# Performance work log

Measured on AMD Instinct MI355X. Metric: run time of the kernel, lower is better.

The kernel has to match this reference:

```python
import jax, jax.numpy as jnp
import numpy as np

B, T, D, H, LORA = 4, 1024, 1024, 16, 64
HD = D // H
BLOCK_ID, N_BLOCKS = 6, 12


def _ln(x, w, b, eps=1e-5):
    m = x.mean(-1, keepdims=True)
    v = ((x - m) ** 2).mean(-1, keepdims=True)
    return (x - m) * jax.lax.rsqrt(v + eps) * w + b


def _lora(z, a, b, l):
    return l + jnp.tanh(z @ a.T) @ b.T


def setup_inputs() -> dict:
    key = jax.random.key(0)
    ks = iter(jax.random.split(key, 64))
    rn = lambda shape, s: jax.random.normal(next(ks), shape, jnp.float32) * s
    inp = {}
    inp['x'] = rn((B, T, D), 1.0)
    r1 = 1.0 - BLOCK_ID / N_BLOCKS
    i = np.arange(D)
    inp['xw'] = jnp.asarray(1.0 - (i / D) ** r1, jnp.float32)
    for nm in ('rW', 'kW', 'vW', 'gW'):
        inp[nm] = rn((D, D), 0.02)
    for p in ('r', 'k', 'v', 'g', 'd'):
        inp[p + '_la'] = rn((LORA, D), 0.001)
        inp[p + '_lb'] = rn((D, LORA), 0.001)
        inp[p + '_ll'] = rn((D,), 1.0)
    inp['ln_w'] = jnp.full((HD,), ((1 + BLOCK_ID) / N_BLOCKS) ** 0.7, jnp.float32)
    inp['ln_b'] = jnp.zeros((HD,), jnp.float32)
    inp['oW'] = rn((D, D), 0.02)
    inp['init_state'] = rn((H, HD, HD), 1.0)
    r0 = BLOCK_ID / (N_BLOCKS - 1)
    ih = i % HD
    inp['u'] = jnp.asarray(r0 * (1 - ih / (D - 1)) + np.remainder(0.1 * (ih + 1), 3.0), jnp.float32)
    return inp


def reference(x, xw, rW, kW, vW, gW, r_la, r_lb, r_ll, k_la, k_lb, k_ll,
              v_la, v_lb, v_ll, g_la, g_lb, g_ll, d_la, d_lb, d_ll,
              ln_w, ln_b, oW, init_state, u):
    b, t, d = x.shape
    h = init_state.shape[0]
    hd = d // h
    # token shift: xx[t] = x[t-1], xx[0] = 0
    xx = jnp.concatenate([jnp.zeros_like(x[:, :1]), x[:, :-1]], axis=1)
    dx = xx - x
    lerpx = x + dx * xw
    r = (x + dx * _lora(lerpx, r_la, r_lb, r_ll)) @ rW.T
    k = (x + dx * _lora(lerpx, k_la, k_lb, k_ll)) @ kW.T
    v = (x + dx * _lora(lerpx, v_la, v_lb, v_ll)) @ vW.T
    g = (x + dx * _lora(lerpx, g_la, g_lb, g_ll)) @ gW.T
    w = jnp.exp(-jnp.exp(_lora(x + dx * _lora(lerpx, d_la, d_lb, d_ll), d_la, d_lb, d_ll)))
    # [B,T,D] -> [T,B,H,hd] for the time scan
    split = lambda z: z.reshape(b, t, h, hd).transpose(1, 0, 2, 3)
    rs, ws, ks, vs = split(r), split(w), split(k), split(v)
    uh = u.reshape(h, hd)
    st0 = jnp.broadcast_to(init_state, (b, h, hd, hd))

    def step(st, inp):
        rt, wt, kt, vt = inp
        kv = jnp.einsum('bhi,bhj->bhij', kt, vt)      # outer product
        y = jnp.einsum('bhi,bhij->bhj', rt, st + uh[None, :, :, None] * kv)
        return wt[..., None] * st + kv, y             # diag(w) @ S + kv

    st1, ys = jax.lax.scan(step, st0, (rs, ws, ks, vs))  # ys: [T,B,H,hd]
    o = jax.nn.silu(g.reshape(b, t, h, hd)) * _ln(ys.transpose(1, 0, 2, 3), ln_w, ln_b)
    return o.reshape(b, t, d) @ oW.T, st1
```

## Files before the change

### kernel.cpp

```cpp
#include <hip/hip_runtime.h>
#include <hip/hip_bf16.h>

typedef unsigned short u16;
typedef unsigned int u32;
typedef __attribute__((ext_vector_type(4))) float f32x4;
typedef __attribute__((ext_vector_type(8))) short s16x8;

#define AS1 __attribute__((address_space(1)))
#define AS3 __attribute__((address_space(3)))

#define NB 4
#define TTOK 1024
#define DD 1024
#define NH 16
#define HD 64
#define MT 4096
#define NCH 16
#define CLEN 64

static __device__ __forceinline__ float b2f(u16 u) {
  union { unsigned int u; float f; } c; c.u = ((unsigned int)u) << 16; return c.f;
}
static __device__ __forceinline__ float ubit(u32 u) {
  union { u32 u; float f; } c; c.u = u; return c.f;
}
static __device__ __forceinline__ u16 f2b(float f) {
  union { float f; unsigned int u; } c; c.f = f;
  return (u16)((c.u + 0x7fffu + ((c.u >> 16) & 1u)) >> 16);
}
static __device__ __forceinline__ void gload16(const u16* g, u16* l) {
  __builtin_amdgcn_global_load_lds((const AS1 u32*)g, (AS3 u32*)l, 16, 0, 0);
}
static __device__ __forceinline__ int swz(int lin) {
  return lin ^ (((lin >> 9) & 3) << 5) ^ (((lin >> 7) & 1) << 4);
}

__global__ __launch_bounds__(256) void convW(const float* __restrict__ s0, const float* __restrict__ s1,
                                             const float* __restrict__ s2, const float* __restrict__ s3,
                                             const float* __restrict__ s4, u16* __restrict__ dst) {
  long f = ((long)blockIdx.x * 256 + threadIdx.x) << 2;
  int sel = (int)(f >> 20);
  const float* s = sel == 0 ? s0 : sel == 1 ? s1 : sel == 2 ? s2 : sel == 3 ? s3 : s4;
  long off = f & 1048575;
  f32x4 v = *(const f32x4*)&s[off];
  ushort4 o; o.x = f2b(v[0]); o.y = f2b(v[1]); o.z = f2b(v[2]); o.w = f2b(v[3]);
  *(ushort4*)&dst[f] = o;
}

__global__ __launch_bounds__(256) void convLora(
    const float* a0, const float* a1, const float* a2, const float* a3, const float* a4,
    const float* b0, const float* b1, const float* b2, const float* b3, const float* b4,
    const float* l0, const float* l1, const float* l2, const float* l3, const float* l4,
    u16* __restrict__ laD, u16* __restrict__ lbD, float* __restrict__ llD) {
  long f = ((long)blockIdx.x * 256 + threadIdx.x) << 2;
  if (f < 327680) {
    int sel = (int)(f >> 16); long off = f & 65535;
    const float* s = sel == 0 ? a0 : sel == 1 ? a1 : sel == 2 ? a2 : sel == 3 ? a3 : a4;
    f32x4 v = *(const f32x4*)&s[off];
    ushort4 o; o.x = f2b(v[0]); o.y = f2b(v[1]); o.z = f2b(v[2]); o.w = f2b(v[3]);
    *(ushort4*)&laD[f] = o;
  } else if (f < 655360) {
    long g = f - 327680;
    int sel = (int)(g >> 16); long off = g & 65535;
    const float* s = sel == 0 ? b0 : sel == 1 ? b1 : sel == 2 ? b2 : sel == 3 ? b3 : b4;
    f32x4 v = *(const f32x4*)&s[off];
    ushort4 o; o.x = f2b(v[0]); o.y = f2b(v[1]); o.z = f2b(v[2]); o.w = f2b(v[3]);
    *(ushort4*)&lbD[g] = o;
  } else if (f < 660480) {
    long g = f - 655360;
    int sel = (int)(g >> 10); long off = g & 1023;
    const float* s = sel == 0 ? l0 : sel == 1 ? l1 : sel == 2 ? l2 : sel == 3 ? l3 : l4;
    *(f32x4*)&llD[g] = *(const f32x4*)&s[off];
  }
}

__global__ __launch_bounds__(256) void prep(const float* __restrict__ x, const float* __restrict__ xw,
                                            u16* __restrict__ lerpx, u16* __restrict__ xB,
                                            u16* __restrict__ dxB) {
  long f = ((long)blockIdx.x * 256 + threadIdx.x) << 2;
  int d = (int)(f & (DD - 1));
  int m = (int)(f >> 10);
  int t = m & (TTOK - 1);
  f32x4 xv = *(const f32x4*)&x[f];
  f32x4 xm = {};
  if (t > 0) xm = *(const f32x4*)&x[f - DD];
  f32x4 xwv = *(const f32x4*)&xw[d];
  f32x4 dx = xm - xv;
  f32x4 lp = xv + dx * xwv;
  ushort4 o; o.x = f2b(lp[0]); o.y = f2b(lp[1]); o.z = f2b(lp[2]); o.w = f2b(lp[3]);
  *(ushort4*)&lerpx[f] = o;
  ushort4 ox; ox.x = f2b(xv[0]); ox.y = f2b(xv[1]); ox.z = f2b(xv[2]); ox.w = f2b(xv[3]);
  *(ushort4*)&xB[f] = ox;
  ushort4 od; od.x = f2b(dx[0]); od.y = f2b(dx[1]); od.z = f2b(dx[2]); od.w = f2b(dx[3]);
  *(ushort4*)&dxB[f] = od;
}

template<int BM, int BN, int EPI>
__launch_bounds__(256)
__global__ void gemm2(const u16* __restrict__ Ab, long sAz,
                      const u16* __restrict__ Bb, long sBz,
                      void* __restrict__ Ob, long sOz,
                      const float* __restrict__ llb,
                      const u16* __restrict__ xB,
                      const u16* __restrict__ dxB,
                      int M, int N, int K) {
  __shared__ __align__(16) u16 As[BM * 64];
  __shared__ __align__(16) u16 Bs[BN * 64];
  const int z = blockIdx.z;
  const u16* A = Ab + (long)z * sAz;
  const u16* Bw = Bb + (long)z * sBz;
  const int m0 = blockIdx.y * BM;
  const int n0 = blockIdx.x * BN;
  const int tid = threadIdx.x;
  const int l = tid & 63;
  const int wv = tid >> 6;
  constexpr int WM = BM / 2, WN = BN / 2;
  constexpr int FM = WM / 16, FN = WN / 16;
  const int wm0 = (wv >> 1) * WM, wn0 = (wv & 1) * WN;
  const int lrow = l & 15, lk = (l >> 4) * 8;
  constexpr int GA = BM / 32, GB = BN / 32;
  int gA[GA], gB[GB];
#pragma unroll
  for (int q = 0; q < GA; ++q) {
    int d = (q * 256 + tid) * 16;
    int bb = swz(d);
    gA[q] = (m0 + (bb >> 7)) * K + ((bb & 127) >> 1);
  }
#pragma unroll
  for (int q = 0; q < GB; ++q) {
    int d = (q * 256 + tid) * 16;
    int bb = swz(d);
    gB[q] = (n0 + (bb >> 7)) * K + ((bb & 127) >> 1);
  }
  int aOff[FM][2], bOff[FN][2];
#pragma unroll
  for (int m = 0; m < FM; ++m)
#pragma unroll
    for (int kk = 0; kk < 2; ++kk)
      aOff[m][kk] = swz(((wm0 + m * 16 + lrow) << 7) + (kk << 6) + (lk << 1));
#pragma unroll
  for (int n = 0; n < FN; ++n)
#pragma unroll
    for (int kk = 0; kk < 2; ++kk)
      bOff[n][kk] = swz(((wn0 + n * 16 + lrow) << 7) + (kk << 6) + (lk << 1));
  f32x4 acc[FM][FN] = {};
  for (int k0 = 0; k0 < K; k0 += 64) {
    __syncthreads();
#pragma unroll
    for (int q = 0; q < GA; ++q)
      gload16(&A[(long)gA[q] + k0], (u16*)((char*)As + (q * 256 + tid) * 16));
#pragma unroll
    for (int q = 0; q < GB; ++q)
      gload16(&Bw[(long)gB[q] + k0], (u16*)((char*)Bs + (q * 256 + tid) * 16));
    __syncthreads();
#pragma unroll
    for (int kk = 0; kk < 2; ++kk) {
      s16x8 af[FM], bfr[FN];
#pragma unroll
      for (int m = 0; m < FM; ++m) af[m] = *(const s16x8*)((const char*)As + aOff[m][kk]);
#pragma unroll
      for (int n = 0; n < FN; ++n) bfr[n] = *(const s16x8*)((const char*)Bs + bOff[n][kk]);
#pragma unroll
      for (int m = 0; m < FM; ++m)
#pragma unroll
        for (int n = 0; n < FN; ++n)
          acc[m][n] = __builtin_amdgcn_mfma_f32_16x16x32_bf16(af[m], bfr[n], acc[m][n], 0, 0, 0);
    }
  }
#pragma unroll
  for (int m = 0; m < FM; ++m) {
#pragma unroll
    for (int n = 0; n < FN; ++n) {
      const int j = n0 + wn0 + n * 16 + lrow;
#pragma unroll
      for (int q = 0; q < 4; ++q) {
        const int i = m0 + wm0 + m * 16 + (l >> 4) * 4 + q;
        const long off = (long)i * N + j;
        float v = acc[m][n][q];
        if constexpr (EPI == 0) {
          ((float*)Ob + (long)z * sOz)[off] = v;
        } else if constexpr (EPI == 1) {
          ((u16*)Ob + (long)z * sOz)[off] = f2b(tanhf(v));
        } else if constexpr (EPI == 2) {
          float val = b2f(xB[off]) + b2f(dxB[off]) * (llb[(long)z * N + j] + v);
          ((u16*)Ob + (long)z * sOz)[off] = f2b(val);
        } else if constexpr (EPI == 3) {
          ((float*)Ob + (long)z * sOz)[off] = expf(-expf(llb[j] + v));
        } else {
          ((u16*)Ob + (long)z * sOz)[off] = f2b(v);
        }
      }
    }
  }
}

__global__ __launch_bounds__(256) void scan_local(
    const u16* __restrict__ rP, const u16* __restrict__ kP,
    const u16* __restrict__ vP, const float* __restrict__ wP,
    const float* __restrict__ uP,
    float* __restrict__ ys0, float* __restrict__ ys1,
    float* __restrict__ ys2, float* __restrict__ ys3,
    u16* __restrict__ rtil, float* __restrict__ SL, float* __restrict__ AC) {
  const int bhc = blockIdx.x;
  const int c = bhc & (NCH - 1), h = (bhc >> 4) & (NH - 1), b = bhc >> 8;
  const int j = threadIdx.x & 63;
  const int qu = __builtin_amdgcn_readfirstlane(threadIdx.x >> 6);
  const int so = qu * 16;
  float s[16];
#pragma unroll
  for (int x = 0; x < 16; ++x) s[x] = 0.f;
  long base = ((long)(b * TTOK + c * CLEN) << 10) + h * HD;
  float* __restrict__ ysel = qu == 0 ? ys0 : qu == 1 ? ys1 : qu == 2 ? ys2 : ys3;

  u32 rc[8], kc[8]; float wc[16];
#pragma unroll
  for (int e = 0; e < 8; ++e) {
    rc[e] = *(const u32*)(rP + base + so + 2 * e);
    kc[e] = *(const u32*)(kP + base + so + 2 * e);
  }
#pragma unroll
  for (int e = 0; e < 16; ++e) wc[e] = wP[base + so + e];

  float Aj = 1.f;
  const float uj = uP[h * HD + j];
  float vjc = b2f(vP[base + j]);
  float rjv = 0.f, kjv = 0.f, wjv = 0.f;
  if (qu == 0) { rjv = b2f(rP[base + j]); kjv = b2f(kP[base + j]); wjv = wP[base + j]; }

  for (int tt = 0; tt < CLEN; ++tt) {
    const long nb = base + DD;
    u32 rn_[8], kn_[8]; float wn_[16];
#pragma unroll
    for (int e = 0; e < 8; ++e) {
      rn_[e] = *(const u32*)(rP + nb + so + 2 * e);
      kn_[e] = *(const u32*)(kP + nb + so + 2 * e);
    }
#pragma unroll
    for (int e = 0; e < 16; ++e) wn_[e] = wP[nb + so + e];
    float vjn = b2f(vP[nb + j]);
    float rjn = 0.f, kjn = 0.f, wjn = 0.f;
    if (qu == 0) { rjn = b2f(rP[nb + j]); kjn = b2f(kP[nb + j]); wjn = wP[nb + j]; }

    float ya = 0.f, yb = 0.f;
#pragma unroll
    for (int e = 0; e < 8; ++e) {
      const float r0 = ubit(rc[e] << 16), r1 = ubit(rc[e] & 0xffff0000u);
      const float k0 = ubit(kc[e] << 16), k1 = ubit(kc[e] & 0xffff0000u);
      ya = fmaf(r0, s[2 * e], ya);
      s[2 * e] = fmaf(wc[2 * e], s[2 * e], k0 * vjc);
      yb = fmaf(r1, s[2 * e + 1], yb);
      s[2 * e + 1] = fmaf(wc[2 * e + 1], s[2 * e + 1], k1 * vjc);
    }
    float y = ya + yb;
    if (qu == 0) {
      rtil[base + j] = f2b(rjv * Aj);
      float al = rjv * uj * kjv;
#pragma unroll
      for (int msk = 1; msk < 64; msk <<= 1) al += __shfl_xor(al, msk, 64);
      y = fmaf(al, vjc, y);
      Aj *= wjv;
      rjv = rjn; kjv = kjn; wjv = wjn;
    }
    ysel[base + j] = y;
    base = nb; vjc = vjn;
#pragma unroll
    for (int e = 0; e < 8; ++e) { rc[e] = rn_[e]; kc[e] = kn_[e]; }
#pragma unroll
    for (int e = 0; e < 16; ++e) wc[e] = wn_[e];
  }
#pragma unroll
  for (int x = 0; x < 16; ++x)
    SL[((long)bhc * 64 + so + x) * 64 + j] = s[x];
  if (qu == 0) AC[(long)bhc * 64 + j] = Aj;
}

__global__ __launch_bounds__(256) void scan_prop(
    float* __restrict__ SL, const float* __restrict__ AC,
    const float* __restrict__ initS, float* __restrict__ st1) {
  const int bh = blockIdx.x >> 2;
  const int jq = blockIdx.x & 3;
  const int h = bh & (NH - 1);
  const int i = threadIdx.x >> 2;
  const int jo = jq * 16 + (threadIdx.x & 3) * 4;
  f32x4 sin4 = *(const f32x4*)(initS + ((long)h * 64 + i) * 64 + jo);
  for (int cc = 0; cc < NCH; ++cc) {
    const long bhc = (long)bh * NCH + cc;
    f32x4* slp = (f32x4*)(SL + (bhc * 64 + i) * 64 + jo);
    const float Ai = AC[bhc * 64 + i];
    f32x4 sl = *slp;
    *slp = sin4;
    sin4 = Ai * sin4 + sl;
  }
  *(f32x4*)(st1 + ((long)bh * 64 + i) * 64 + jo) = sin4;
}

__global__ __launch_bounds__(256) void scan_corr(
    const float* __restrict__ SL, const u16* __restrict__ rtil, float* __restrict__ ys) {
  __shared__ __align__(16) float S[64 * 64];
  const int bhc = blockIdx.x;
  const int c = bhc & (NCH - 1), h = (bhc >> 4) & (NH - 1), b = bhc >> 8;
  const int tid = threadIdx.x;
  const f32x4* sp = (const f32x4*)(SL + (long)bhc * 4096);
  for (int q = tid; q < 1024; q += 256) ((f32x4*)S)[q] = sp[q];
  __syncthreads();
  const int t = tid >> 2, jg = (tid & 3) * 16;
  const long base = ((long)(b * TTOK + c * CLEN + t) * DD) + h * HD;
  f32x4 yacc[4] = {};
  const u16* rp = rtil + base;
#pragma unroll 8
  for (int i = 0; i < 64; ++i) {
    const float r = b2f(rp[i]);
    const f32x4* srow = (const f32x4*)&S[i * 64 + jg];
#pragma unroll
    for (int e = 0; e < 4; ++e) yacc[e] += r * srow[e];
  }
  f32x4* yp = (f32x4*)(ys + base + jg);
#pragma unroll
  for (int e = 0; e < 4; ++e) yp[e] += yacc[e];
}

__global__ __launch_bounds__(256) void ln_silu(
    const float* __restrict__ ys0, const float* __restrict__ ys1,
    const float* __restrict__ ys2, const float* __restrict__ ys3,
    const u16* __restrict__ gP,
    const float* __restrict__ lnw, const float* __restrict__ lnb,
    u16* __restrict__ oB) {
  const int ridx = blockIdx.x * 4 + (threadIdx.x >> 6);
  const int lane = threadIdx.x & 63;
  const long basem = (long)ridx * 64;
  const float y = ys0[basem + lane] + ys1[basem + lane] + ys2[basem + lane] + ys3[basem + lane];
  float su = y, sq = y * y;
#pragma unroll
  for (int msk = 1; msk < 64; msk <<= 1) {
    su += __shfl_xor(su, msk, 64);
    sq += __shfl_xor(sq, msk, 64);
  }
  const float mean = su * (1.f / 64.f);
  const float var = sq * (1.f / 64.f) - mean * mean;
  const float rs = rsqrtf(var + 1e-5f);
  const float g = b2f(gP[basem + lane]);
  const float silu = g / (1.f + expf(-g));
  const float val = silu * ((y - mean) * rs * lnw[lane] + lnb[lane]);
  oB[basem + lane] = f2b(val);
}

extern "C" void kernel_launch(void* const* d_in, const int* in_sizes, int n_in,
                              void* d_out, int out_size, void* d_ws, size_t ws_size,
                              hipStream_t stream) {
  const float* x   = (const float*)d_in[0];
  const float* xw  = (const float*)d_in[1];
  const float* rW  = (const float*)d_in[2];
  const float* kW  = (const float*)d_in[3];
  const float* vW  = (const float*)d_in[4];
  const float* gW  = (const float*)d_in[5];
  const float* r_la = (const float*)d_in[6],  *r_lb = (const float*)d_in[7],  *r_ll = (const float*)d_in[8];
  const float* k_la = (const float*)d_in[9],  *k_lb = (const float*)d_in[10], *k_ll = (const float*)d_in[11];
  const float* v_la = (const float*)d_in[12], *v_lb = (const float*)d_in[13], *v_ll = (const float*)d_in[14];
  const float* g_la = (const float*)d_in[15], *g_lb = (const float*)d_in[16], *g_ll = (const float*)d_in[17];
  const float* d_la = (const float*)d_in[18], *d_lb = (const float*)d_in[19], *d_ll = (const float*)d_in[20];
  const float* lnw = (const float*)d_in[21];
  const float* lnb = (const float*)d_in[22];
  const float* oW  = (const float*)d_in[23];
  const float* initS = (const float*)d_in[24];
  const float* uP  = (const float*)d_in[25];
  float* out = (float*)d_out;

  char* ws = (char*)d_ws;
  u16*   W_all  = (u16*)(ws + 0);
  u16*   la_all = (u16*)(ws + 10485760);
  u16*   lb_all = (u16*)(ws + 11141120);
  float* ll_all = (float*)(ws + 11796480);
  u16*   lerpx  = (u16*)(ws + 11816960);
  u16*   xB     = (u16*)(ws + 20205568);
  u16*   dxB    = (u16*)(ws + 28594176);
  u16*   t1_all = (u16*)(ws + 36982784);
  u16*   z_all  = (u16*)(ws + 39604224);
  u16*   rkvg   = (u16*)(ws + 81547264);
  float* wbuf   = (float*)(ws + 115101696);
  u16*   rtil   = (u16*)(ws + 131878912);
  float* SL     = (float*)(ws + 140267520);
  float* AC     = (float*)(ws + 157044736);
  float* ys0    = (float*)(ws + 157306880);
  u16*   oB     = (u16*)(ws + 174084096);
  float* ys1    = (float*)(ws + 11816960);
  float* ys2    = (float*)(ws + 39604224);
  float* ys3    = (float*)(ws + 56381440);

  convW<<<5120, 256, 0, stream>>>(rW, kW, vW, gW, oW, W_all);
  convLora<<<645, 256, 0, stream>>>(r_la, k_la, v_la, g_la, d_la,
                                    r_lb, k_lb, v_lb, g_lb, d_lb,
                                    r_ll, k_ll, v_ll, g_ll, d_ll,
                                    la_all, lb_all, ll_all);
  prep<<<4096, 256, 0, stream>>>(x, xw, lerpx, xB, dxB);

  gemm2<64, 64, 1><<<dim3(1, 64, 5), 256, 0, stream>>>(
      lerpx, 0L, la_all, 65536L, (void*)t1_all, 262144L, nullptr, nullptr, nullptr, MT, 64, 1024);
  gemm2<128, 128, 2><<<dim3(8, 32, 5), 256, 0, stream>>>(
      t1_all, 262144L, lb_all, 65536L, (void*)z_all, 4194304L, ll_all, xB, dxB, MT, 1024, 64);
  gemm2<64, 64, 1><<<dim3(1, 64, 1), 256, 0, stream>>>(
      z_all + 4L * 4194304, 0L, la_all + 4L * 65536, 0L, (void*)t1_all, 0L, nullptr, nullptr, nullptr, MT, 64, 1024);
  gemm2<128, 128, 3><<<dim3(8, 32, 1), 256, 0, stream>>>(
      t1_all, 0L, lb_all + 4L * 65536, 0L, (void*)wbuf, 0L, ll_all + 4096, nullptr, nullptr, MT, 1024, 64);
  gemm2<128, 128, 4><<<dim3(8, 32, 4), 256, 0, stream>>>(
      z_all, 4194304L, W_all, 1048576L, (void*)rkvg, 4194304L, nullptr, nullptr, nullptr, MT, 1024, 1024);

  scan_local<<<1024, 256, 0, stream>>>(rkvg, rkvg + 4194304L, rkvg + 2L * 4194304, wbuf,
                                       uP, ys0, ys1, ys2, ys3, rtil, SL, AC);
  scan_prop<<<256, 256, 0, stream>>>(SL, AC, initS, out + 4194304);
  scan_corr<<<1024, 256, 0, stream>>>(SL, rtil, ys0);

  ln_silu<<<16384, 256, 0, stream>>>(ys0, ys1, ys2, ys3, rkvg + 3L * 4194304, lnw, lnb, oB);
  gemm2<128, 128, 0><<<dim3(8, 32, 1), 256, 0, stream>>>(
      oB, 0L, W_all + 4L * 1048576, 0L, (void*)out, 0L, nullptr, nullptr, nullptr, MT, 1024, 1024);
}
```

Baseline: 388.4 us.

## Stage scan chunk inputs in LDS and store partial outputs as bf16

scan_local now copies each chunk's r, k, v and w tiles into shared memory with bulk global-to-LDS loads up front. The time loop then reads them with vector LDS loads instead of per-step register-prefetched global loads. The four per-quarter partial outputs are written as bf16 rather than fp32, and scan_corr writes a separate fp32 correction buffer that ln_silu adds in, replacing the read-modify-write into ys0. This cuts global traffic and per-step load latency in the scan, but bf16 partial sums lose some precision, and the buffers are aliased into reused workspace regions such as wbuf.

```diff
diff --git a/kernel.cpp b/kernel.cpp
--- a/kernel.cpp
+++ b/kernel.cpp
@@ -4,6 +4,7 @@
 typedef unsigned short u16;
 typedef unsigned int u32;
 typedef __attribute__((ext_vector_type(4))) float f32x4;
+typedef __attribute__((ext_vector_type(4))) u32 u32x4;
 typedef __attribute__((ext_vector_type(8))) short s16x8;
 
 #define AS1 __attribute__((address_space(1)))
@@ -198,75 +199,86 @@
     const u16* __restrict__ rP, const u16* __restrict__ kP,
     const u16* __restrict__ vP, const float* __restrict__ wP,
     const float* __restrict__ uP,
-    float* __restrict__ ys0, float* __restrict__ ys1,
-    float* __restrict__ ys2, float* __restrict__ ys3,
+    u16* __restrict__ ys0, u16* __restrict__ ys1,
+    u16* __restrict__ ys2, u16* __restrict__ ys3,
     u16* __restrict__ rtil, float* __restrict__ SL, float* __restrict__ AC) {
+  __shared__ __align__(16) u16 Rs[64 * 64];
+  __shared__ __align__(16) u16 Ks[64 * 64];
+  __shared__ __align__(16) u16 Vs[64 * 64];
+  __shared__ __align__(16) float Ws[64 * 64];
   const int bhc = blockIdx.x;
   const int c = bhc & (NCH - 1), h = (bhc >> 4) & (NH - 1), b = bhc >> 8;
-  const int j = threadIdx.x & 63;
-  const int qu = __builtin_amdgcn_readfirstlane(threadIdx.x >> 6);
+  const int tid = threadIdx.x;
+  const int j = tid & 63;
+  const int qu = tid >> 6;
+  const long base0 = ((long)(b * TTOK + c * CLEN) << 10) + h * HD;
+#pragma unroll
+  for (int q = 0; q < 2; ++q) {
+    int cidx = q * 256 + tid;
+    int t = cidx >> 3, off = (cidx & 7) * 8;
+    gload16(&rP[base0 + (long)t * DD + off], (u16*)Rs + cidx * 8);
+    gload16(&kP[base0 + (long)t * DD + off], (u16*)Ks + cidx * 8);
+    gload16(&vP[base0 + (long)t * DD + off], (u16*)Vs + cidx * 8);
+  }
+#pragma unroll
+  for (int q = 0; q < 4; ++q) {
+    int cidx = q * 256 + tid;
+    int t = cidx >> 4, off = (cidx & 15) * 4;
+    __builtin_amdgcn_global_load_lds((const AS1 u32*)&wP[base0 + (long)t * DD + off],
+                                     (AS3 u32*)((float*)Ws + cidx * 4), 16, 0, 0);
+  }
+  __syncthreads();
   const int so = qu * 16;
   float s[16];
 #pragma unroll
   for (int x = 0; x < 16; ++x) s[x] = 0.f;
-  long base = ((long)(b * TTOK + c * CLEN) << 10) + h * HD;
-  float* __restrict__ ysel = qu == 0 ? ys0 : qu == 1 ? ys1 : qu == 2 ? ys2 : ys3;
-
-  u32 rc[8], kc[8]; float wc[16];
-#pragma unroll
-  for (int e = 0; e < 8; ++e) {
-    rc[e] = *(const u32*)(rP + base + so + 2 * e);
-    kc[e] = *(const u32*)(kP + base + so + 2 * e);
-  }
-#pragma unroll
-  for (int e = 0; e < 16; ++e) wc[e] = wP[base + so + e];
-
   float Aj = 1.f;
   const float uj = uP[h * HD + j];
-  float vjc = b2f(vP[base + j]);
-  float rjv = 0.f, kjv = 0.f, wjv = 0.f;
-  if (qu == 0) { rjv = b2f(rP[base + j]); kjv = b2f(kP[base + j]); wjv = wP[base + j]; }
-
+  long base = base0;
+  u16* __restrict__ ysel = qu == 0 ? ys0 : qu == 1 ? ys1 : qu == 2 ? ys2 : ys3;
   for (int tt = 0; tt < CLEN; ++tt) {
-    const long nb = base + DD;
-    u32 rn_[8], kn_[8]; float wn_[16];
-#pragma unroll
-    for (int e = 0; e < 8; ++e) {
-      rn_[e] = *(const u32*)(rP + nb + so + 2 * e);
-      kn_[e] = *(const u32*)(kP + nb + so + 2 * e);
+    const int ro = tt * 64 + so;
+    u32x4 ra = *(const u32x4*)&Rs[ro];
+    u32x4 rb = *(const u32x4*)&Rs[ro + 8];
+    u32x4 ka = *(const u32x4*)&Ks[ro];
+    u32x4 kb = *(const u32x4*)&Ks[ro + 8];
+    float wl[16];
+#pragma unroll
+    for (int e = 0; e < 4; ++e) *(f32x4*)&wl[e * 4] = *(const f32x4*)&Ws[ro + e * 4];
+    const float vj = b2f(Vs[tt * 64 + j]);
+    float ya = 0.f, yb = 0.f;
+#pragma unroll
+    for (int e = 0; e < 4; ++e) {
+      const float r0 = ubit(ra[e] << 16), r1 = ubit(ra[e] & 0xffff0000u);
+      const float k0 = ubit(ka[e] << 16), k1 = ubit(ka[e] & 0xffff0000u);
+      ya = fmaf(r0, s[2 * e], ya);
+      s[2 * e] = fmaf(wl[2 * e], s[2 * e], k0 * vj);
+      yb = fmaf(r1, s[2 * e + 1], yb);
+      s[2 * e + 1] = fmaf(wl[2 * e + 1], s[2 * e + 1], k1 * vj);
     }
 #pragma unroll
-    for (int e = 0; e < 16; ++e) wn_[e] = wP[nb + so + e];
-    float vjn = b2f(vP[nb + j]);
-    float rjn = 0.f, kjn = 0.f, wjn = 0.f;
-    if (qu == 0) { rjn = b2f(rP[nb + j]); kjn = b2f(kP[nb + j]); wjn = wP[nb + j]; }
-
-    float ya = 0.f, yb = 0.f;
-#pragma unroll
-    for (int e = 0; e < 8; ++e) {
-      const float r0 = ubit(rc[e] << 16), r1 = ubit(rc[e] & 0xffff0000u);
-      const float k0 = ubit(kc[e] << 16), k1 = ubit(kc[e] & 0xffff0000u);
-      ya = fmaf(r0, s[2 * e], ya);
-      s[2 * e] = fmaf(wc[2 * e], s[2 * e], k0 * vjc);
-      yb = fmaf(r1, s[2 * e + 1], yb);
-      s[2 * e + 1] = fmaf(wc[2 * e + 1], s[2 * e + 1], k1 * vjc);
+    for (int e = 0; e < 4; ++e) {
+      const float r0 = ubit(rb[e] << 16), r1 = ubit(rb[e] & 0xffff0000u);
+      const float k0 = ubit(kb[e] << 16), k1 = ubit(kb[e] & 0xffff0000u);
+      ya = fmaf(r0, s[8 + 2 * e], ya);
+      s[8 + 2 * e] = fmaf(wl[8 + 2 * e], s[8 + 2 * e], k0 * vj);
+      yb = fmaf(r1, s[8 + 2 * e + 1], yb);
+      s[8 + 2 * e + 1] = fmaf(wl[8 + 2 * e + 1], s[8 + 2 * e + 1], k1 * vj);
     }
     float y = ya + yb;
     if (qu == 0) {
-      rtil[base + j] = f2b(rjv * Aj);
-      float al = rjv * uj * kjv;
+      const float rj = b2f(Rs[tt * 64 + j]);
+      const float kj = b2f(Ks[tt * 64 + j]);
+      const float wj = Ws[tt * 64 + j];
+      rtil[base + j] = f2b(rj * Aj);
+      float al = rj * uj * kj;
 #pragma unroll
       for (int msk = 1; msk < 64; msk <<= 1) al += __shfl_xor(al, msk, 64);
-      y = fmaf(al, vjc, y);
-      Aj *= wjv;
-      rjv = rjn; kjv = kjn; wjv = wjn;
+      y = fmaf(al, vj, y);
+      Aj *= wj;
     }
-    ysel[base + j] = y;
-    base = nb; vjc = vjn;
-#pragma unroll
-    for (int e = 0; e < 8; ++e) { rc[e] = rn_[e]; kc[e] = kn_[e]; }
-#pragma unroll
-    for (int e = 0; e < 16; ++e) wc[e] = wn_[e];
+    ysel[base + j] = f2b(y);
+    base += DD;
   }
 #pragma unroll
   for (int x = 0; x < 16; ++x)
@@ -295,7 +307,7 @@
 }
 
 __global__ __launch_bounds__(256) void scan_corr(
-    const float* __restrict__ SL, const u16* __restrict__ rtil, float* __restrict__ ys) {
+    const float* __restrict__ SL, const u16* __restrict__ rtil, float* __restrict__ ysC) {
   __shared__ __align__(16) float S[64 * 64];
   const int bhc = blockIdx.x;
   const int c = bhc & (NCH - 1), h = (bhc >> 4) & (NH - 1), b = bhc >> 8;
@@ -314,21 +326,23 @@
 #pragma unroll
     for (int e = 0; e < 4; ++e) yacc[e] += r * srow[e];
   }
-  f32x4* yp = (f32x4*)(ys + base + jg);
-#pragma unroll
-  for (int e = 0; e < 4; ++e) yp[e] += yacc[e];
+  f32x4* yp = (f32x4*)(ysC + base + jg);
+#pragma unroll
+  for (int e = 0; e < 4; ++e) yp[e] = yacc[e];
 }
 
 __global__ __launch_bounds__(256) void ln_silu(
-    const float* __restrict__ ys0, const float* __restrict__ ys1,
-    const float* __restrict__ ys2, const float* __restrict__ ys3,
+    const u16* __restrict__ p0, const u16* __restrict__ p1,
+    const u16* __restrict__ p2, const u16* __restrict__ p3,
+    const float* __restrict__ ysC,
     const u16* __restrict__ gP,
     const float* __restrict__ lnw, const float* __restrict__ lnb,
     u16* __restrict__ oB) {
   const int ridx = blockIdx.x * 4 + (threadIdx.x >> 6);
   const int lane = threadIdx.x & 63;
   const long basem = (long)ridx * 64;
-  const float y = ys0[basem + lane] + ys1[basem + lane] + ys2[basem + lane] + ys3[basem + lane];
+  const float y = b2f(p0[basem + lane]) + b2f(p1[basem + lane]) +
+                  b2f(p2[basem + lane]) + b2f(p3[basem + lane]) + ysC[basem + lane];
   float su = y, sq = y * y;
 #pragma unroll
   for (int msk = 1; msk < 64; msk <<= 1) {
@@ -380,11 +394,12 @@
   u16*   rtil   = (u16*)(ws + 131878912);
   float* SL     = (float*)(ws + 140267520);
   float* AC     = (float*)(ws + 157044736);
-  float* ys0    = (float*)(ws + 157306880);
+  u16*   ys0p   = (u16*)(ws + 157306880);
   u16*   oB     = (u16*)(ws + 174084096);
-  float* ys1    = (float*)(ws + 11816960);
-  float* ys2    = (float*)(ws + 39604224);
-  float* ys3    = (float*)(ws + 56381440);
+  u16*   ys1p   = (u16*)(ws + 11816960);
+  u16*   ys2p   = (u16*)(ws + 39604224);
+  u16*   ys3p   = (u16*)(ws + 47992832);
+  float* ysC    = (float*)(ws + 115101696);
 
   convW<<<5120, 256, 0, stream>>>(rW, kW, vW, gW, oW, W_all);
   convLora<<<645, 256, 0, stream>>>(r_la, k_la, v_la, g_la, d_la,
@@ -405,11 +420,11 @@
       z_all, 4194304L, W_all, 1048576L, (void*)rkvg, 4194304L, nullptr, nullptr, nullptr, MT, 1024, 1024);
 
   scan_local<<<1024, 256, 0, stream>>>(rkvg, rkvg + 4194304L, rkvg + 2L * 4194304, wbuf,
-                                       uP, ys0, ys1, ys2, ys3, rtil, SL, AC);
+                                       uP, ys0p, ys1p, ys2p, ys3p, rtil, SL, AC);
   scan_prop<<<256, 256, 0, stream>>>(SL, AC, initS, out + 4194304);
-  scan_corr<<<1024, 256, 0, stream>>>(SL, rtil, ys0);
-
-  ln_silu<<<16384, 256, 0, stream>>>(ys0, ys1, ys2, ys3, rkvg + 3L * 4194304, lnw, lnb, oB);
+  scan_corr<<<1024, 256, 0, stream>>>(SL, rtil, ysC);
+
+  ln_silu<<<16384, 256, 0, stream>>>(ys0p, ys1p, ys2p, ys3p, ysC, rkvg + 3L * 4194304, lnw, lnb, oB);
   gemm2<128, 128, 0><<<dim3(8, 32, 1), 256, 0, stream>>>(
       oB, 0L, W_all + 4L * 1048576, 0L, (void*)out, 0L, nullptr, nullptr, nullptr, MT, 1024, 1024);
 }
```

Result: faster. 368.4 us (-5.1%).
